# Optimization experiments

Measured on AMD Instinct MI355X. Metric: run time of the kernel, lower is better.

The kernel has to match this reference:

```python
import jax, jax.numpy as jnp
import numpy as np

N = 100000      # nodes
E = 1600000     # edges (no self-loops by construction)
DIN, DH, DOUT = 128, 128, 64
EPS = 1e-8      # torch cosine_similarity eps
LN_EPS = 1e-5


def _segsum(v, idx, n=N):
    return jax.ops.segment_sum(v, idx, num_segments=n)


def att_coef(feats, row, col):
    """Edge-wise cosine-sim attention + degree norm + self-loop append (torch no_grad block).
    Returns fixed-shape (row2, col2, vals2) of length E+N; filtered edges get weight 0
    (equivalent to removal for all scatter_add / message-passing math)."""
    dot = jnp.einsum('ed,ed->e', feats[row], feats[col])            # [E]
    nrm = jnp.maximum(jnp.linalg.norm(feats, axis=1), EPS)          # [N]
    sims = dot / (nrm[row] * nrm[col])
    keep = sims >= 0.1                                              # row!=col guaranteed
    sims = jnp.where(keep, sims, 0.0)
    deg = _segsum(sims, row)
    dinv = jnp.where(deg > 0, deg ** -0.5, 0.0)                     # inf -> 0
    sims = dinv[row] * sims * dinv[col]
    deg_new = _segsum(keep.astype(feats.dtype), col) + 1.0          # [N], >= 1
    self_val = 1.0 / deg_new
    vals = jnp.where(keep, jnp.exp(sims), 0.0)                      # removed edges -> 0
    sl = jnp.arange(N)
    row2 = jnp.concatenate([row, sl])
    col2 = jnp.concatenate([col, sl])
    vals2 = jnp.concatenate([vals, jnp.exp(self_val)])
    return row2, col2, vals2


def gcn_conv(x, row, col, w, W, b):
    """PyG GCNConv (normalize=True, add_self_loops=False) with given edge_weight."""
    h = x @ W                                                        # [N, out]
    deg = _segsum(w, col)
    dinv = jnp.where(deg > 0, deg ** -0.5, 0.0)
    norm = dinv[row] * w * dinv[col]                                 # [E+N]
    out = _segsum(norm[:, None] * h[row], col)                       # scatter to targets
    return out + b


def layer_norm(x, g, b):
    mu = jnp.mean(x, axis=-1, keepdims=True)
    var = jnp.mean((x - mu) ** 2, axis=-1, keepdims=True)
    return (x - mu) * jax.lax.rsqrt(var + LN_EPS) * g + b


def setup_inputs() -> dict:
    key = jax.random.key(0)
    ks = jax.random.split(key, 6)
    x = jax.random.normal(ks[0], (N, DIN), jnp.float32)
    row = jax.random.randint(ks[1], (E,), 0, N)
    col = jax.random.randint(ks[2], (E,), 0, N)
    col = jnp.where(col == row, (col + 1) % N, col)                  # no self-loops
    s1 = float(np.sqrt(6.0 / (DIN + DH)))                            # glorot
    s2 = float(np.sqrt(6.0 / (DH + DOUT)))
    W1 = jax.random.uniform(ks[3], (DIN, DH), jnp.float32, -s1, s1)
    W2 = jax.random.uniform(ks[4], (DH, DOUT), jnp.float32, -s2, s2)
    return dict(x=x, row=row, col=col,
                W1=W1, b1=jnp.zeros((DH,), jnp.float32),
                ln_g=jnp.ones((DH,), jnp.float32), ln_b=jnp.zeros((DH,), jnp.float32),
                W2=W2, b2=jnp.zeros((DOUT,), jnp.float32))


def reference(x, row, col, W1, b1, ln_g, ln_b, W2, b2):
    # layer 1: att_coef (no_grad) -> GCNConv -> LayerNorm -> ReLU (dropout is eval no-op)
    r2, c2, v2 = att_coef(jax.lax.stop_gradient(x), row, col)
    h = gcn_conv(x, r2, c2, v2, W1, b1)
    h = jax.nn.relu(layer_norm(h, ln_g, ln_b))
    # layer 2: att_coef on updated features (original edge list), final conv + log_softmax
    r2, c2, v2 = att_coef(jax.lax.stop_gradient(h), row, col)
    out = gcn_conv(h, r2, c2, v2, W2, b2)
    return jax.nn.log_softmax(out, axis=-1)
```

## Files before the change

kernel.cpp:

```cpp
#include <hip/hip_runtime.h>
#include <math.h>

#define EPSF 1e-8f
#define LN_EPS 1e-5f
#define BL_MARGIN 0.002f

#define BKT_SH 8
#define NBKT 512
#define CHUNK 2048
#define BCAP 5120

typedef unsigned int  u32;
typedef unsigned short u16;
typedef _Float16 h2_t __attribute__((ext_vector_type(2)));
typedef _Float16 half8_t __attribute__((ext_vector_type(8)));
typedef float f32x4_t __attribute__((ext_vector_type(4)));

static __device__ inline u32 pack_h2(float a, float b) {
    h2_t h; h.x = (_Float16)a; h.y = (_Float16)b;
    return __builtin_bit_cast(u32, h);
}
static __device__ inline float h2lo(u32 u) {
    return (float)__builtin_bit_cast(h2_t, u).x;
}
static __device__ inline float h2hi(u32 u) {
    return (float)__builtin_bit_cast(h2_t, u).y;
}

static __device__ inline f32x4_t mfma16(uint4 a, uint4 b, f32x4_t c) {
    return __builtin_amdgcn_mfma_f32_16x16x32_f16(
        __builtin_bit_cast(half8_t, a), __builtin_bit_cast(half8_t, b), c, 0, 0, 0);
}
static __device__ inline float sel4(f32x4_t a, int m) {
    return m == 0 ? a[0] : m == 1 ? a[1] : m == 2 ? a[2] : a[3];
}

__global__ __launch_bounds__(256) void cast_norm_k(const float* __restrict__ feat,
    u32* __restrict__ fhf, float* __restrict__ nrm, float* __restrict__ deg1, int n) {
    int wid  = (blockIdx.x * 256 + threadIdx.x) >> 6;
    int lane = threadIdx.x & 63;
    if (wid >= n) return;
    float2 v = *(const float2*)(feat + (size_t)wid * 128 + lane * 2);
    float s = v.x * v.x + v.y * v.y;
    #pragma unroll
    for (int off = 32; off; off >>= 1) s += __shfl_xor(s, off, 64);
    float nv = fmaxf(sqrtf(s), EPSF);
    float inv = 1.0f / nv;
    fhf[(size_t)wid * 64 + lane] = pack_h2(v.x * inv, v.y * inv);
    if (lane == 0) { nrm[wid] = nv; deg1[wid] = 0.0f; }
}


__global__ __launch_bounds__(256) void binfill_k(const int* __restrict__ row,
    const int* __restrict__ col, int* __restrict__ bcur,
    int2* __restrict__ ebuf, int ecnt) {
    __shared__ int lc[NBKT], ls[NBKT], cur[NBKT], gbase[NBKT];
    __shared__ int2 pairs[CHUNK];
    __shared__ int dstv[CHUNK];
    int t = threadIdx.x;
    int e0 = blockIdx.x * CHUNK;
    int m = min(CHUNK, ecnt - e0);
    lc[t] = 0; lc[t + 256] = 0; cur[t] = 0; cur[t + 256] = 0;
    __syncthreads();
    int myc[CHUNK / 256], myr[CHUNK / 256];
    #pragma unroll
    for (int i = 0; i < CHUNK / 256; ++i) {
        int idx = t + i * 256;
        if (idx < m) {
            myc[i] = col[e0 + idx];
            myr[i] = row[e0 + idx];
            atomicAdd(&lc[myc[i] >> BKT_SH], 1);
        }
    }
    __syncthreads();
    int v0 = lc[t], v1 = lc[t + 256];
    ls[t] = v0; ls[t + 256] = v1; __syncthreads();
    for (int off = 1; off < 256; off <<= 1) {
        int a0 = (t >= off) ? ls[t - off] : 0;
        int a1 = (t >= off) ? ls[256 + t - off] : 0;
        __syncthreads();
        ls[t] += a0; ls[t + 256] += a1;
        __syncthreads();
    }
    int h0 = ls[255];
    int e0x = ls[t] - v0;
    int e1x = ls[t + 256] - v1 + h0;
    __syncthreads();
    ls[t] = e0x; ls[t + 256] = e1x;
    if (v0) gbase[t] = atomicAdd(&bcur[t], v0);
    if (v1) gbase[t + 256] = atomicAdd(&bcur[t + 256], v1);
    __syncthreads();
    #pragma unroll
    for (int i = 0; i < CHUNK / 256; ++i) {
        int idx = t + i * 256;
        if (idx < m) {
            int b = myc[i] >> BKT_SH;
            int s = ls[b] + atomicAdd(&cur[b], 1);
            pairs[s] = make_int2(myc[i], myr[i]);
            int pos = gbase[b] + (s - ls[b]);
            dstv[s]  = (pos < BCAP) ? (b * BCAP + pos) : -1;
        }
    }
    __syncthreads();
    for (int s = t; s < m; s += 256) {
        int d = dstv[s];
        if (d >= 0) ebuf[d] = pairs[s];
    }
}

__global__ __launch_bounds__(256) void bucket_csr_k(const int2* __restrict__ ebuf,
    const int* __restrict__ bcur, int* __restrict__ startAll,
    int* __restrict__ cntAll, int* __restrict__ rowAll, int* __restrict__ colAll,
    int n) {
    __shared__ int sc[NBKT];
    __shared__ int cnt[256], lst[256], cur[256];
    __shared__ int rowbuf[BCAP];
    int b = blockIdx.x, t = threadIdx.x;
    int c0 = b << BKT_SH;
    int s0v = min(bcur[t], BCAP), s1v = min(bcur[t + 256], BCAP);
    sc[t] = s0v; sc[t + 256] = s1v; __syncthreads();
    for (int off = 1; off < 256; off <<= 1) {
        int a0 = (t >= off) ? sc[t - off] : 0;
        int a1 = (t >= off) ? sc[256 + t - off] : 0;
        __syncthreads();
        sc[t] += a0; sc[t + 256] += a1;
        __syncthreads();
    }
    int m  = min(bcur[b], BCAP);
    int g0 = ((b >= 256) ? sc[255] : 0) + sc[b] - m;
    size_t ebase = (size_t)b * BCAP;
    cnt[t] = 0; cur[t] = 0;
    __syncthreads();
    for (int i = t; i < m; i += 256)
        atomicAdd(&cnt[ebuf[ebase + i].x - c0], 1);
    __syncthreads();
    int v = cnt[t];
    lst[t] = v; __syncthreads();
    for (int off = 1; off < 256; off <<= 1) {
        int a = (t >= off) ? lst[t - off] : 0;
        __syncthreads();
        lst[t] += a;
        __syncthreads();
    }
    int ex = lst[t] - v;
    __syncthreads();
    lst[t] = ex;
    __syncthreads();
    int c = c0 + t;
    if (c < n) { startAll[c] = g0 + lst[t]; cntAll[c] = cnt[t]; }
    for (int i = t; i < m; i += 256) {
        int2 p = ebuf[ebase + i];
        int ci = p.x - c0;
        int pos = lst[ci] + atomicAdd(&cur[ci], 1);
        rowbuf[pos] = p.y;
    }
    __syncthreads();
    for (int i = t; i < m; i += 256)
        rowAll[g0 + i] = rowbuf[i];
    __syncthreads();
    {
        int base = lst[t], cn = cnt[t], cc = c0 + t;
        for (int k2 = 0; k2 < cn; ++k2) rowbuf[base + k2] = cc;
    }
    __syncthreads();
    for (int i = t; i < m; i += 256)
        colAll[g0 + i] = rowbuf[i];
}

__global__ __launch_bounds__(256) void edge_dot_flat_k(const u32* __restrict__ fhf,
    const float* __restrict__ feat32, const int* __restrict__ rowAll,
    const int* __restrict__ colAll, const float* __restrict__ nrm,
    float* __restrict__ sims, float* __restrict__ deg1, int ecnt) {
    int wv   = (blockIdx.x * 256 + threadIdx.x) >> 6;
    int lane = threadIdx.x & 63;
    int e0 = wv * 32;
    if (e0 >= ecnt) return;
    int lr = lane & 15, kq = lane >> 4;
    bool diag = (kq == (lr >> 2));
    int m3 = lane & 3;
    int em1 = ecnt - 1;

    int e1 = e0 + lr, e2 = e0 + 16 + lr;
    int e1c = min(e1, em1), e2c = min(e2, em1);
    int r1 = rowAll[e1c], c1 = colAll[e1c];
    int r2 = rowAll[e2c], c2 = colAll[e2c];
    const u32* pa1 = fhf + (size_t)c1 * 64 + kq * 4;
    const u32* pb1 = fhf + (size_t)r1 * 64 + kq * 4;
    const u32* pa2 = fhf + (size_t)c2 * 64 + kq * 4;
    const u32* pb2 = fhf + (size_t)r2 * 64 + kq * 4;
    uint4 a10 = *(const uint4*)(pa1);
    uint4 a11 = *(const uint4*)(pa1 + 16);
    uint4 a12 = *(const uint4*)(pa1 + 32);
    uint4 a13 = *(const uint4*)(pa1 + 48);
    uint4 b10 = *(const uint4*)(pb1);
    uint4 b11 = *(const uint4*)(pb1 + 16);
    uint4 b12 = *(const uint4*)(pb1 + 32);
    uint4 b13 = *(const uint4*)(pb1 + 48);
    uint4 a20 = *(const uint4*)(pa2);
    uint4 a21 = *(const uint4*)(pa2 + 16);
    uint4 a22 = *(const uint4*)(pa2 + 32);
    uint4 a23 = *(const uint4*)(pa2 + 48);
    uint4 b20 = *(const uint4*)(pb2);
    uint4 b21 = *(const uint4*)(pb2 + 16);
    uint4 b22 = *(const uint4*)(pb2 + 32);
    uint4 b23 = *(const uint4*)(pb2 + 48);

    f32x4_t acc1 = {0.f, 0.f, 0.f, 0.f};
    acc1 = mfma16(a10, b10, acc1);
    acc1 = mfma16(a11, b11, acc1);
    acc1 = mfma16(a12, b12, acc1);
    acc1 = mfma16(a13, b13, acc1);
    f32x4_t acc2 = {0.f, 0.f, 0.f, 0.f};
    acc2 = mfma16(a20, b20, acc2);
    acc2 = mfma16(a21, b21, acc2);
    acc2 = mfma16(a22, b22, acc2);
    acc2 = mfma16(a23, b23, acc2);

    float p1 = sel4(acc1, m3);
    float p2 = sel4(acc2, m3);
    bool act1 = diag && (e1 < ecnt);
    bool act2 = diag && (e2 < ecnt);

    unsigned long long bl = __ballot(act1 && fabsf(p1 - 0.1f) < BL_MARGIN);
    while (bl) {
        int src = __ffsll((unsigned long long)bl) - 1; bl &= bl - 1ull;
        int rt = __shfl(r1, src, 64);
        int ct = __shfl(c1, src, 64);
        float2 xa = *(const float2*)(feat32 + (size_t)rt * 128 + lane * 2);
        float2 xb = *(const float2*)(feat32 + (size_t)ct * 128 + lane * 2);
        float s2 = xa.x * xb.x + xa.y * xb.y;
        #pragma unroll
        for (int off = 32; off; off >>= 1) s2 += __shfl_xor(s2, off, 64);
        float pf = s2 / (nrm[rt] * nrm[ct]);
        if (lane == src) p1 = pf;
    }
    unsigned long long bl2 = __ballot(act2 && fabsf(p2 - 0.1f) < BL_MARGIN);
    while (bl2) {
        int src = __ffsll((unsigned long long)bl2) - 1; bl2 &= bl2 - 1ull;
        int rt = __shfl(r2, src, 64);
        int ct = __shfl(c2, src, 64);
        float2 xa = *(const float2*)(feat32 + (size_t)rt * 128 + lane * 2);
        float2 xb = *(const float2*)(feat32 + (size_t)ct * 128 + lane * 2);
        float s2 = xa.x * xb.x + xa.y * xb.y;
        #pragma unroll
        for (int off = 32; off; off >>= 1) s2 += __shfl_xor(s2, off, 64);
        float pf = s2 / (nrm[rt] * nrm[ct]);
        if (lane == src) p2 = pf;
    }
    if (act1) {
        float kv = (p1 >= 0.1f) ? p1 : 0.0f;
        sims[e1] = kv;
        if (kv > 0.0f) atomicAdd(&deg1[r1], kv);
    }
    if (act2) {
        float kv = (p2 >= 0.1f) ? p2 : 0.0f;
        sims[e2] = kv;
        if (kv > 0.0f) atomicAdd(&deg1[r2], kv);
    }
}

__global__ __launch_bounds__(256) void edge_c_csr_k(const float* __restrict__ sims,
    const int* __restrict__ rowAll, const int* __restrict__ startAll,
    const int* __restrict__ cntAll, const float* __restrict__ deg1,
    int2* __restrict__ kv, int* __restrict__ cntK, float* __restrict__ dinv2,
    float* __restrict__ cself, int n) {
    int wid  = (blockIdx.x * 256 + threadIdx.x) >> 6;
    int lane = threadIdx.x & 63;
    if (wid >= n) return;
    int s0 = startAll[wid], cnt = cntAll[wid];
    float degc = deg1[wid];
    float d1c = (degc > 0.0f) ? 1.0f / sqrtf(degc) : 0.0f;
    float vsum = 0.0f; int kc = 0;
    for (int jj = 0; jj < cnt; jj += 64) {
        int j = jj + lane;
        bool keep = false; int r = 0; float v = 0.0f;
        if (j < cnt) {
            float s = sims[s0 + j];
            if (s > 0.0f) {
                r = rowAll[s0 + j];
                float dr = 1.0f / sqrtf(deg1[r]);
                v = expf(dr * s * d1c);
                keep = true;
            }
        }
        unsigned long long m = __ballot(keep ? 1 : 0);
        if (keep) {
            int pre = __popcll(m & ((1ull << lane) - 1ull));
            int2 pk; pk.x = r; pk.y = __float_as_int(v);
            kv[s0 + kc + pre] = pk;
            vsum += v;
        }
        kc += __popcll(m);
    }
    #pragma unroll
    for (int off = 32; off; off >>= 1) vsum += __shfl_xor(vsum, off, 64);
    if (lane == 0) {
        float ws_ = expf(1.0f / ((float)kc + 1.0f));
        float dg = ws_ + vsum;
        float di = 1.0f / sqrtf(dg);
        dinv2[wid] = di;
        cself[wid] = di * ws_;
        cntK[wid]  = kc;
    }
}


__global__ __launch_bounds__(256) void gemm128_k(const float* __restrict__ A,
    const float* __restrict__ W, const float* __restrict__ scale,
    float* __restrict__ out, int n) {
    __shared__ float Ws[128 * 128];
    for (int i = threadIdx.x; i < 128 * 128 / 4; i += 256)
        ((float4*)Ws)[i] = ((const float4*)W)[i];
    __syncthreads();
    const int TPN = 32;
    int group = threadIdx.x / TPN;
    int tin   = threadIdx.x % TPN;
    int nid   = (blockIdx.x * 8 + group) * 4;
    if (nid >= n) return;
    int dbase = tin * 4;
    int nm1 = n - 1;
    const float4* a0 = (const float4*)(A + (size_t)min(nid,     nm1) * 128);
    const float4* a1 = (const float4*)(A + (size_t)min(nid + 1, nm1) * 128);
    const float4* a2 = (const float4*)(A + (size_t)min(nid + 2, nm1) * 128);
    const float4* a3 = (const float4*)(A + (size_t)min(nid + 3, nm1) * 128);
    float4 acc0 = {0,0,0,0}, acc1 = {0,0,0,0}, acc2 = {0,0,0,0}, acc3 = {0,0,0,0};
    #pragma unroll 2
    for (int k4 = 0; k4 < 32; ++k4) {
        const float* wr = Ws + (k4 * 4) * 128 + dbase;
        float4 w0 = *(const float4*)(wr);
        float4 w1 = *(const float4*)(wr + 128);
        float4 w2 = *(const float4*)(wr + 256);
        float4 w3 = *(const float4*)(wr + 384);
        float4 v0 = a0[k4], v1 = a1[k4], v2 = a2[k4], v3 = a3[k4];
        acc0.x += v0.x*w0.x + v0.y*w1.x + v0.z*w2.x + v0.w*w3.x;
        acc0.y += v0.x*w0.y + v0.y*w1.y + v0.z*w2.y + v0.w*w3.y;
        acc0.z += v0.x*w0.z + v0.y*w1.z + v0.z*w2.z + v0.w*w3.z;
        acc0.w += v0.x*w0.w + v0.y*w1.w + v0.z*w2.w + v0.w*w3.w;
        acc1.x += v1.x*w0.x + v1.y*w1.x + v1.z*w2.x + v1.w*w3.x;
        acc1.y += v1.x*w0.y + v1.y*w1.y + v1.z*w2.y + v1.w*w3.y;
        acc1.z += v1.x*w0.z + v1.y*w1.z + v1.z*w2.z + v1.w*w3.z;
        acc1.w += v1.x*w0.w + v1.y*w1.w + v1.z*w2.w + v1.w*w3.w;
        acc2.x += v2.x*w0.x + v2.y*w1.x + v2.z*w2.x + v2.w*w3.x;
        acc2.y += v2.x*w0.y + v2.y*w1.y + v2.z*w2.y + v2.w*w3.y;
        acc2.z += v2.x*w0.z + v2.y*w1.z + v2.z*w2.z + v2.w*w3.z;
        acc2.w += v2.x*w0.w + v2.y*w1.w + v2.z*w2.w + v2.w*w3.w;
        acc3.x += v3.x*w0.x + v3.y*w1.x + v3.z*w2.x + v3.w*w3.x;
        acc3.y += v3.x*w0.y + v3.y*w1.y + v3.z*w2.y + v3.w*w3.y;
        acc3.z += v3.x*w0.z + v3.y*w1.z + v3.z*w2.z + v3.w*w3.z;
        acc3.w += v3.x*w0.w + v3.y*w1.w + v3.z*w2.w + v3.w*w3.w;
    }
    float4 accs[4] = {acc0, acc1, acc2, acc3};
    #pragma unroll
    for (int i = 0; i < 4; ++i) {
        if (nid + i < n) {
            float sc = scale[nid + i];
            float4 r; r.x = accs[i].x * sc; r.y = accs[i].y * sc;
            r.z = accs[i].z * sc; r.w = accs[i].w * sc;
            *(float4*)(out + (size_t)(nid + i) * 128 + dbase) = r;
        }
    }
}

__global__ __launch_bounds__(256) void gemm64_hf_k(const float* __restrict__ A,
    const float* __restrict__ W, const float* __restrict__ scale,
    u32* __restrict__ outhf, int n) {
    __shared__ float Ws[128 * 64];
    for (int i = threadIdx.x; i < 128 * 64 / 4; i += 256)
        ((float4*)Ws)[i] = ((const float4*)W)[i];
    __syncthreads();
    const int TPN = 16;
    int group = threadIdx.x / TPN;
    int tin   = threadIdx.x % TPN;
    int nid   = (blockIdx.x * 16 + group) * 4;
    if (nid >= n) return;
    int dbase = tin * 4;
    int nm1 = n - 1;
    const float4* a0 = (const float4*)(A + (size_t)min(nid,     nm1) * 128);
    const float4* a1 = (const float4*)(A + (size_t)min(nid + 1, nm1) * 128);
    const float4* a2 = (const float4*)(A + (size_t)min(nid + 2, nm1) * 128);
    const float4* a3 = (const float4*)(A + (size_t)min(nid + 3, nm1) * 128);
    float4 acc0 = {0,0,0,0}, acc1 = {0,0,0,0}, acc2 = {0,0,0,0}, acc3 = {0,0,0,0};
    #pragma unroll 2
    for (int k4 = 0; k4 < 32; ++k4) {
        const float* wr = Ws + (k4 * 4) * 64 + dbase;
        float4 w0 = *(const float4*)(wr);
        float4 w1 = *(const float4*)(wr + 64);
        float4 w2 = *(const float4*)(wr + 128);
        float4 w3 = *(const float4*)(wr + 192);
        float4 v0 = a0[k4], v1 = a1[k4], v2 = a2[k4], v3 = a3[k4];
        acc0.x += v0.x*w0.x + v0.y*w1.x + v0.z*w2.x + v0.w*w3.x;
        acc0.y += v0.x*w0.y + v0.y*w1.y + v0.z*w2.y + v0.w*w3.y;
        acc0.z += v0.x*w0.z + v0.y*w1.z + v0.z*w2.z + v0.w*w3.z;
        acc0.w += v0.x*w0.w + v0.y*w1.w + v0.z*w2.w + v0.w*w3.w;
        acc1.x += v1.x*w0.x + v1.y*w1.x + v1.z*w2.x + v1.w*w3.x;
        acc1.y += v1.x*w0.y + v1.y*w1.y + v1.z*w2.y + v1.w*w3.y;
        acc1.z += v1.x*w0.z + v1.y*w1.z + v1.z*w2.z + v1.w*w3.z;
        acc1.w += v1.x*w0.w + v1.y*w1.w + v1.z*w2.w + v1.w*w3.w;
        acc2.x += v2.x*w0.x + v2.y*w1.x + v2.z*w2.x + v2.w*w3.x;
        acc2.y += v2.x*w0.y + v2.y*w1.y + v2.z*w2.y + v2.w*w3.y;
        acc2.z += v2.x*w0.z + v2.y*w1.z + v2.z*w2.z + v2.w*w3.z;
        acc2.w += v2.x*w0.w + v2.y*w1.w + v2.z*w2.w + v2.w*w3.w;
        acc3.x += v3.x*w0.x + v3.y*w1.x + v3.z*w2.x + v3.w*w3.x;
        acc3.y += v3.x*w0.y + v3.y*w1.y + v3.z*w2.y + v3.w*w3.y;
        acc3.z += v3.x*w0.z + v3.y*w1.z + v3.z*w2.z + v3.w*w3.z;
        acc3.w += v3.x*w0.w + v3.y*w1.w + v3.z*w2.w + v3.w*w3.w;
    }
    float4 accs[4] = {acc0, acc1, acc2, acc3};
    #pragma unroll
    for (int i = 0; i < 4; ++i) {
        if (nid + i < n) {
            float sc = scale[nid + i];
            u32 o0 = pack_h2(accs[i].x * sc, accs[i].y * sc);
            u32 o1 = pack_h2(accs[i].z * sc, accs[i].w * sc);
            *(uint2*)(outhf + (size_t)(nid + i) * 32 + tin * 2)
                = make_uint2(o0, o1);
        }
    }
}


__global__ __launch_bounds__(256) void gather_ln_k(const float* __restrict__ hs,
    const int2* __restrict__ kv, const int* __restrict__ startAll,
    const int* __restrict__ cntK, const float* __restrict__ dinv2,
    const float* __restrict__ cself, const float* __restrict__ bias,
    const float* __restrict__ g, const float* __restrict__ bln,
    float* __restrict__ outbuf, u32* __restrict__ outhf,
    float* __restrict__ nrm, float* __restrict__ deg1, int n) {
    int wid = (blockIdx.x * 256 + threadIdx.x) >> 5;
    int l   = threadIdx.x & 31;
    if (wid >= n) return;
    int s0 = startAll[wid], k = cntK[wid];
    if (l == 0) deg1[wid] = 0.0f;
    float4 acc = {0,0,0,0};
    int km1 = s0 + k - 1;
    for (int j0 = 0; j0 < k; j0 += 8) {
        int2 p[8];
        #pragma unroll
        for (int i = 0; i < 8; ++i) p[i] = kv[min(s0 + j0 + i, km1)];
        float4 h[8];
        #pragma unroll
        for (int i = 0; i < 8; ++i)
            h[i] = *(const float4*)(hs + (size_t)p[i].x * 128 + l * 4);
        #pragma unroll
        for (int i = 0; i < 8; ++i) {
            float v = (j0 + i < k) ? __int_as_float(p[i].y) : 0.0f;
            acc.x += v * h[i].x; acc.y += v * h[i].y;
            acc.z += v * h[i].z; acc.w += v * h[i].w;
        }
    }
    float di = dinv2[wid], cs = cself[wid];
    float4 hsv = *(const float4*)(hs + (size_t)wid * 128 + l * 4);
    float4 vb  = *(const float4*)(bias + l * 4);
    float x0 = di*acc.x + cs*hsv.x + vb.x;
    float x1 = di*acc.y + cs*hsv.y + vb.y;
    float x2 = di*acc.z + cs*hsv.z + vb.z;
    float x3 = di*acc.w + cs*hsv.w + vb.w;
    float s = x0 + x1 + x2 + x3;
    #pragma unroll
    for (int off = 16; off; off >>= 1) s += __shfl_xor(s, off, 64);
    float mu = s * (1.0f / 128.0f);
    float d0 = x0 - mu, d1 = x1 - mu, d2 = x2 - mu, d3 = x3 - mu;
    float vv = d0*d0 + d1*d1 + d2*d2 + d3*d3;
    #pragma unroll
    for (int off = 16; off; off >>= 1) vv += __shfl_xor(vv, off, 64);
    float rstd = 1.0f / sqrtf(vv * (1.0f / 128.0f) + LN_EPS);
    float4 vg  = *(const float4*)(g + l * 4);
    float4 vbl = *(const float4*)(bln + l * 4);
    float y0 = fmaxf(d0 * rstd * vg.x + vbl.x, 0.0f);
    float y1 = fmaxf(d1 * rstd * vg.y + vbl.y, 0.0f);
    float y2 = fmaxf(d2 * rstd * vg.z + vbl.z, 0.0f);
    float y3 = fmaxf(d3 * rstd * vg.w + vbl.w, 0.0f);
    float4 yo; yo.x = y0; yo.y = y1; yo.z = y2; yo.w = y3;
    *(float4*)(outbuf + (size_t)wid * 128 + l * 4) = yo;
    float ns = y0*y0 + y1*y1 + y2*y2 + y3*y3;
    #pragma unroll
    for (int off = 16; off; off >>= 1) ns += __shfl_xor(ns, off, 64);
    float nv = fmaxf(sqrtf(ns), EPSF);
    float inv = 1.0f / nv;
    uint2 oh; oh.x = pack_h2(y0 * inv, y1 * inv); oh.y = pack_h2(y2 * inv, y3 * inv);
    *(uint2*)(outhf + (size_t)wid * 64 + l * 2) = oh;
    if (l == 0) nrm[wid] = nv;
}

__global__ __launch_bounds__(256) void gather_lsm_hf_k(const u32* __restrict__ g2s,
    const int2* __restrict__ kv, const int* __restrict__ startAll,
    const int* __restrict__ cntK, const float* __restrict__ dinv2,
    const float* __restrict__ cself, const float* __restrict__ b2,
    float* __restrict__ out, int n) {
    int wid = (blockIdx.x * 256 + threadIdx.x) >> 5;
    int l   = threadIdx.x & 31;
    if (wid >= n) return;
    int s0 = startAll[wid], k = cntK[wid];
    float acc0 = 0.f, acc1 = 0.f;
    int km1 = s0 + k - 1;
    for (int j0 = 0; j0 < k; j0 += 8) {
        int2 p[8];
        #pragma unroll
        for (int i = 0; i < 8; ++i) p[i] = kv[min(s0 + j0 + i, km1)];
        u32 gv[8];
        #pragma unroll
        for (int i = 0; i < 8; ++i) gv[i] = g2s[(size_t)p[i].x * 32 + l];
        #pragma unroll
        for (int i = 0; i < 8; ++i) {
            float v = (j0 + i < k) ? __int_as_float(p[i].y) : 0.0f;
            acc0 += v * h2lo(gv[i]); acc1 += v * h2hi(gv[i]);
        }
    }
    float di = dinv2[wid], cs = cself[wid];
    u32 gsu = g2s[(size_t)wid * 32 + l];
    float2 vb = *(const float2*)(b2 + l * 2);
    float v0 = di * acc0 + cs * h2lo(gsu) + vb.x;
    float v1 = di * acc1 + cs * h2hi(gsu) + vb.y;
    float m = fmaxf(v0, v1);
    #pragma unroll
    for (int off = 16; off; off >>= 1) m = fmaxf(m, __shfl_xor(m, off, 64));
    float e = expf(v0 - m) + expf(v1 - m);
    #pragma unroll
    for (int off = 16; off; off >>= 1) e += __shfl_xor(e, off, 64);
    float lse = m + logf(e);
    *(float2*)(out + (size_t)wid * 64 + l * 2) = make_float2(v0 - lse, v1 - lse);
}


extern "C" void kernel_launch(void* const* d_in, const int* in_sizes, int n_in,
                              void* d_out, int out_size, void* d_ws, size_t ws_size,
                              hipStream_t stream) {
    (void)n_in; (void)out_size; (void)ws_size;
    const float* x   = (const float*)d_in[0];
    const int*   row = (const int*)d_in[1];
    const int*   col = (const int*)d_in[2];
    const float* W1  = (const float*)d_in[3];
    const float* b1  = (const float*)d_in[4];
    const float* lng = (const float*)d_in[5];
    const float* lnb = (const float*)d_in[6];
    const float* W2  = (const float*)d_in[7];
    const float* b2  = (const float*)d_in[8];
    float* out = (float*)d_out;

    const int N = in_sizes[0] / 128;
    const int E = in_sizes[1];

    int*   cntAll   = (int*)d_ws;
    int*   startAll = cntAll + N;
    int*   bcur     = startAll + N;
    float* nrm      = (float*)(bcur + 1024);
    float* deg1     = nrm + N;
    float* dinv2    = deg1 + N;
    float* cself    = dinv2 + N;
    int*   cntK     = (int*)(cself + N);
    int*   rowAll   = cntK + N;
    int*   colAll   = rowAll + E;
    int2*  kvp      = (int2*)(colAll + E);
    u32*   fhf      = (u32*)(kvp + E);
    u32*   g2shf    = fhf + (size_t)64 * N;
    float* big      = (float*)(g2shf + (size_t)32 * N);
    float* sims     = big;
    float* hs       = big;
    float* h2       = big + (size_t)128 * N;
    int2*  ebuf     = (int2*)big;

    const int waveBlocks  = (N + 3) / 4;
    const int halfBlocks  = (N + 7) / 8;
    const int flatBlocks  = (E + 127) / 128;
    const int NB          = (N + 255) >> 8;

    hipMemsetAsync(bcur, 0, NBKT * sizeof(int), stream);
    binfill_k<<<(E + CHUNK - 1) / CHUNK, 256, 0, stream>>>(row, col, bcur, ebuf, E);
    bucket_csr_k<<<NB, 256, 0, stream>>>(ebuf, bcur, startAll, cntAll, rowAll,
                                         colAll, N);

    cast_norm_k<<<waveBlocks, 256, 0, stream>>>(x, fhf, nrm, deg1, N);
    edge_dot_flat_k<<<flatBlocks, 256, 0, stream>>>(fhf, x, rowAll, colAll, nrm,
                                                    sims, deg1, E);
    edge_c_csr_k<<<waveBlocks, 256, 0, stream>>>(sims, rowAll, startAll, cntAll, deg1,
                                                 kvp, cntK, dinv2, cself, N);
    gemm128_k<<<(N + 31) / 32, 256, 0, stream>>>(x, W1, dinv2, hs, N);
    gather_ln_k<<<halfBlocks, 256, 0, stream>>>(hs, kvp, startAll, cntK, dinv2, cself,
                                                b1, lng, lnb, h2, fhf, nrm, deg1, N);

    edge_dot_flat_k<<<flatBlocks, 256, 0, stream>>>(fhf, h2, rowAll, colAll, nrm,
                                                    sims, deg1, E);
    edge_c_csr_k<<<waveBlocks, 256, 0, stream>>>(sims, rowAll, startAll, cntAll, deg1,
                                                 kvp, cntK, dinv2, cself, N);
    gemm64_hf_k<<<(N + 63) / 64, 256, 0, stream>>>(h2, W2, dinv2, g2shf, N);
    gather_lsm_hf_k<<<halfBlocks, 256, 0, stream>>>(g2shf, kvp, startAll, cntK, dinv2,
                                                    cself, b2, out, N);
}
```

Baseline: 603.3 us.

## Co-schedule feature GEMMs with edge-dot kernels and defer source-degree scaling to gathers

Each layer's dense GEMM now runs inside the edge cosine-similarity kernel, with blocks interleaved by a ratio, so the GEMM no longer waits for the degree normalization. Because of that, the per-source dinv scaling is moved out of the GEMM and into the gather kernels, which read dinv2 per neighbor. The interleaved key/value array is split into separate row and weight arrays, with the weights stored in place over sims. The GEMM reads W straight from global/L1 instead of staging it in LDS. The cost is extra per-neighbor dinv loads in the gathers and mixed block types sharing one launch.

```diff
diff --git a/kernel.cpp b/kernel.cpp
--- a/kernel.cpp
+++ b/kernel.cpp
@@ -49,7 +49,6 @@
     fhf[(size_t)wid * 64 + lane] = pack_h2(v.x * inv, v.y * inv);
     if (lane == 0) { nrm[wid] = nv; deg1[wid] = 0.0f; }
 }
-
 
 __global__ __launch_bounds__(256) void binfill_k(const int* __restrict__ row,
     const int* __restrict__ col, int* __restrict__ bcur,
@@ -167,13 +166,12 @@
         colAll[g0 + i] = rowbuf[i];
 }
 
-__global__ __launch_bounds__(256) void edge_dot_flat_k(const u32* __restrict__ fhf,
+static __device__ inline void edge_dot_body(int ewk, const u32* __restrict__ fhf,
     const float* __restrict__ feat32, const int* __restrict__ rowAll,
     const int* __restrict__ colAll, const float* __restrict__ nrm,
     float* __restrict__ sims, float* __restrict__ deg1, int ecnt) {
-    int wv   = (blockIdx.x * 256 + threadIdx.x) >> 6;
     int lane = threadIdx.x & 63;
-    int e0 = wv * 32;
+    int e0 = (ewk * 4 + (int)(threadIdx.x >> 6)) * 32;
     if (e0 >= ecnt) return;
     int lr = lane & 15, kq = lane >> 4;
     bool diag = (kq == (lr >> 2));
@@ -259,63 +257,13 @@
     }
 }
 
-__global__ __launch_bounds__(256) void edge_c_csr_k(const float* __restrict__ sims,
-    const int* __restrict__ rowAll, const int* __restrict__ startAll,
-    const int* __restrict__ cntAll, const float* __restrict__ deg1,
-    int2* __restrict__ kv, int* __restrict__ cntK, float* __restrict__ dinv2,
-    float* __restrict__ cself, int n) {
-    int wid  = (blockIdx.x * 256 + threadIdx.x) >> 6;
-    int lane = threadIdx.x & 63;
-    if (wid >= n) return;
-    int s0 = startAll[wid], cnt = cntAll[wid];
-    float degc = deg1[wid];
-    float d1c = (degc > 0.0f) ? 1.0f / sqrtf(degc) : 0.0f;
-    float vsum = 0.0f; int kc = 0;
-    for (int jj = 0; jj < cnt; jj += 64) {
-        int j = jj + lane;
-        bool keep = false; int r = 0; float v = 0.0f;
-        if (j < cnt) {
-            float s = sims[s0 + j];
-            if (s > 0.0f) {
-                r = rowAll[s0 + j];
-                float dr = 1.0f / sqrtf(deg1[r]);
-                v = expf(dr * s * d1c);
-                keep = true;
-            }
-        }
-        unsigned long long m = __ballot(keep ? 1 : 0);
-        if (keep) {
-            int pre = __popcll(m & ((1ull << lane) - 1ull));
-            int2 pk; pk.x = r; pk.y = __float_as_int(v);
-            kv[s0 + kc + pre] = pk;
-            vsum += v;
-        }
-        kc += __popcll(m);
-    }
-    #pragma unroll
-    for (int off = 32; off; off >>= 1) vsum += __shfl_xor(vsum, off, 64);
-    if (lane == 0) {
-        float ws_ = expf(1.0f / ((float)kc + 1.0f));
-        float dg = ws_ + vsum;
-        float di = 1.0f / sqrtf(dg);
-        dinv2[wid] = di;
-        cself[wid] = di * ws_;
-        cntK[wid]  = kc;
-    }
-}
-
-
-__global__ __launch_bounds__(256) void gemm128_k(const float* __restrict__ A,
-    const float* __restrict__ W, const float* __restrict__ scale,
-    float* __restrict__ out, int n) {
-    __shared__ float Ws[128 * 128];
-    for (int i = threadIdx.x; i < 128 * 128 / 4; i += 256)
-        ((float4*)Ws)[i] = ((const float4*)W)[i];
-    __syncthreads();
+
+static __device__ inline void gemm128_body(int gid, const float* __restrict__ A,
+    const float* __restrict__ W, float* __restrict__ out, int n) {
     const int TPN = 32;
     int group = threadIdx.x / TPN;
     int tin   = threadIdx.x % TPN;
-    int nid   = (blockIdx.x * 8 + group) * 4;
+    int nid   = (gid * 8 + group) * 4;
     if (nid >= n) return;
     int dbase = tin * 4;
     int nm1 = n - 1;
@@ -323,14 +271,14 @@
     const float4* a1 = (const float4*)(A + (size_t)min(nid + 1, nm1) * 128);
     const float4* a2 = (const float4*)(A + (size_t)min(nid + 2, nm1) * 128);
     const float4* a3 = (const float4*)(A + (size_t)min(nid + 3, nm1) * 128);
+    const float4* Wv = (const float4*)W;
     float4 acc0 = {0,0,0,0}, acc1 = {0,0,0,0}, acc2 = {0,0,0,0}, acc3 = {0,0,0,0};
     #pragma unroll 2
     for (int k4 = 0; k4 < 32; ++k4) {
-        const float* wr = Ws + (k4 * 4) * 128 + dbase;
-        float4 w0 = *(const float4*)(wr);
-        float4 w1 = *(const float4*)(wr + 128);
-        float4 w2 = *(const float4*)(wr + 256);
-        float4 w3 = *(const float4*)(wr + 384);
+        float4 w0 = Wv[(k4 * 4 + 0) * 32 + tin];
+        float4 w1 = Wv[(k4 * 4 + 1) * 32 + tin];
+        float4 w2 = Wv[(k4 * 4 + 2) * 32 + tin];
+        float4 w3 = Wv[(k4 * 4 + 3) * 32 + tin];
         float4 v0 = a0[k4], v1 = a1[k4], v2 = a2[k4], v3 = a3[k4];
         acc0.x += v0.x*w0.x + v0.y*w1.x + v0.z*w2.x + v0.w*w3.x;
         acc0.y += v0.x*w0.y + v0.y*w1.y + v0.z*w2.y + v0.w*w3.y;
@@ -352,41 +300,31 @@
     float4 accs[4] = {acc0, acc1, acc2, acc3};
     #pragma unroll
     for (int i = 0; i < 4; ++i) {
-        if (nid + i < n) {
-            float sc = scale[nid + i];
-            float4 r; r.x = accs[i].x * sc; r.y = accs[i].y * sc;
-            r.z = accs[i].z * sc; r.w = accs[i].w * sc;
-            *(float4*)(out + (size_t)(nid + i) * 128 + dbase) = r;
-        }
-    }
-}
-
-__global__ __launch_bounds__(256) void gemm64_hf_k(const float* __restrict__ A,
-    const float* __restrict__ W, const float* __restrict__ scale,
-    u32* __restrict__ outhf, int n) {
-    __shared__ float Ws[128 * 64];
-    for (int i = threadIdx.x; i < 128 * 64 / 4; i += 256)
-        ((float4*)Ws)[i] = ((const float4*)W)[i];
-    __syncthreads();
+        if (nid + i < n)
+            *(float4*)(out + (size_t)(nid + i) * 128 + dbase) = accs[i];
+    }
+}
+
+static __device__ inline void gemm64_body(int gid, const float* __restrict__ A,
+    const float* __restrict__ W, u32* __restrict__ outhf, int n) {
     const int TPN = 16;
     int group = threadIdx.x / TPN;
     int tin   = threadIdx.x % TPN;
-    int nid   = (blockIdx.x * 16 + group) * 4;
+    int nid   = (gid * 16 + group) * 4;
     if (nid >= n) return;
-    int dbase = tin * 4;
     int nm1 = n - 1;
     const float4* a0 = (const float4*)(A + (size_t)min(nid,     nm1) * 128);
     const float4* a1 = (const float4*)(A + (size_t)min(nid + 1, nm1) * 128);
     const float4* a2 = (const float4*)(A + (size_t)min(nid + 2, nm1) * 128);
     const float4* a3 = (const float4*)(A + (size_t)min(nid + 3, nm1) * 128);
+    const float4* Wv = (const float4*)W;
     float4 acc0 = {0,0,0,0}, acc1 = {0,0,0,0}, acc2 = {0,0,0,0}, acc3 = {0,0,0,0};
     #pragma unroll 2
     for (int k4 = 0; k4 < 32; ++k4) {
-        const float* wr = Ws + (k4 * 4) * 64 + dbase;
-        float4 w0 = *(const float4*)(wr);
-        float4 w1 = *(const float4*)(wr + 64);
-        float4 w2 = *(const float4*)(wr + 128);
-        float4 w3 = *(const float4*)(wr + 192);
+        float4 w0 = Wv[(k4 * 4 + 0) * 16 + tin];
+        float4 w1 = Wv[(k4 * 4 + 1) * 16 + tin];
+        float4 w2 = Wv[(k4 * 4 + 2) * 16 + tin];
+        float4 w3 = Wv[(k4 * 4 + 3) * 16 + tin];
         float4 v0 = a0[k4], v1 = a1[k4], v2 = a2[k4], v3 = a3[k4];
         acc0.x += v0.x*w0.x + v0.y*w1.x + v0.z*w2.x + v0.w*w3.x;
         acc0.y += v0.x*w0.y + v0.y*w1.y + v0.z*w2.y + v0.w*w3.y;
@@ -409,18 +347,93 @@
     #pragma unroll
     for (int i = 0; i < 4; ++i) {
         if (nid + i < n) {
-            float sc = scale[nid + i];
-            u32 o0 = pack_h2(accs[i].x * sc, accs[i].y * sc);
-            u32 o1 = pack_h2(accs[i].z * sc, accs[i].w * sc);
+            u32 o0 = pack_h2(accs[i].x, accs[i].y);
+            u32 o1 = pack_h2(accs[i].z, accs[i].w);
             *(uint2*)(outhf + (size_t)(nid + i) * 32 + tin * 2)
                 = make_uint2(o0, o1);
         }
     }
 }
 
+__global__ __launch_bounds__(256) void fused1_k(const u32* __restrict__ fhf,
+    const float* __restrict__ x, const int* __restrict__ rowAll,
+    const int* __restrict__ colAll, const float* __restrict__ nrm,
+    float* __restrict__ sims, float* __restrict__ deg1, int ecnt,
+    const float* __restrict__ W1, float* __restrict__ hs, int n,
+    int R, int nGemm) {
+    int b = blockIdx.x;
+    if ((b % R) == 0 && (b / R) < nGemm) {
+        gemm128_body(b / R, x, W1, hs, n);
+    } else {
+        int e = b - min(b / R + 1, nGemm);
+        edge_dot_body(e, fhf, x, rowAll, colAll, nrm, sims, deg1, ecnt);
+    }
+}
+
+__global__ __launch_bounds__(256) void fused2_k(const u32* __restrict__ h2hf,
+    const float* __restrict__ h2, const int* __restrict__ rowAll,
+    const int* __restrict__ colAll, const float* __restrict__ nrm,
+    float* __restrict__ sims, float* __restrict__ deg1, int ecnt,
+    const float* __restrict__ W2, u32* __restrict__ g2shf, int n,
+    int R, int nGemm) {
+    int b = blockIdx.x;
+    if ((b % R) == 0 && (b / R) < nGemm) {
+        gemm64_body(b / R, h2, W2, g2shf, n);
+    } else {
+        int e = b - min(b / R + 1, nGemm);
+        edge_dot_body(e, h2hf, h2, rowAll, colAll, nrm, sims, deg1, ecnt);
+    }
+}
+
+__global__ __launch_bounds__(256) void edge_c_csr_k(float* __restrict__ simsv,
+    const int* __restrict__ rowAll, const int* __restrict__ startAll,
+    const int* __restrict__ cntAll, const float* __restrict__ deg1,
+    int* __restrict__ krow, int* __restrict__ cntK, float* __restrict__ dinv2,
+    float* __restrict__ cself, int n) {
+    int wid  = (blockIdx.x * 256 + threadIdx.x) >> 6;
+    int lane = threadIdx.x & 63;
+    if (wid >= n) return;
+    int s0 = startAll[wid], cnt = cntAll[wid];
+    float degc = deg1[wid];
+    float d1c = (degc > 0.0f) ? 1.0f / sqrtf(degc) : 0.0f;
+    float vsum = 0.0f; int kc = 0;
+    for (int jj = 0; jj < cnt; jj += 64) {
+        int j = jj + lane;
+        bool keep = false; int r = 0; float v = 0.0f;
+        if (j < cnt) {
+            float s = simsv[s0 + j];
+            if (s > 0.0f) {
+                r = rowAll[s0 + j];
+                float dr = 1.0f / sqrtf(deg1[r]);
+                v = expf(dr * s * d1c);
+                keep = true;
+            }
+        }
+        unsigned long long m = __ballot(keep ? 1 : 0);
+        if (keep) {
+            int pre = __popcll(m & ((1ull << lane) - 1ull));
+            simsv[s0 + kc + pre] = v;
+            krow[s0 + kc + pre] = r;
+            vsum += v;
+        }
+        kc += __popcll(m);
+    }
+    #pragma unroll
+    for (int off = 32; off; off >>= 1) vsum += __shfl_xor(vsum, off, 64);
+    if (lane == 0) {
+        float ws_ = expf(1.0f / ((float)kc + 1.0f));
+        float dg = ws_ + vsum;
+        float di = 1.0f / sqrtf(dg);
+        dinv2[wid] = di;
+        cself[wid] = di * ws_;
+        cntK[wid]  = kc;
+    }
+}
+
 
 __global__ __launch_bounds__(256) void gather_ln_k(const float* __restrict__ hs,
-    const int2* __restrict__ kv, const int* __restrict__ startAll,
+    const int* __restrict__ krow, const float* __restrict__ kval,
+    const int* __restrict__ startAll,
     const int* __restrict__ cntK, const float* __restrict__ dinv2,
     const float* __restrict__ cself, const float* __restrict__ bias,
     const float* __restrict__ g, const float* __restrict__ bln,
@@ -434,21 +447,27 @@
     float4 acc = {0,0,0,0};
     int km1 = s0 + k - 1;
     for (int j0 = 0; j0 < k; j0 += 8) {
-        int2 p[8];
-        #pragma unroll
-        for (int i = 0; i < 8; ++i) p[i] = kv[min(s0 + j0 + i, km1)];
+        int ri[8]; float wv[8];
+        #pragma unroll
+        for (int i = 0; i < 8; ++i) {
+            int idx = min(s0 + j0 + i, km1);
+            ri[i] = krow[idx]; wv[i] = kval[idx];
+        }
+        float dv[8];
+        #pragma unroll
+        for (int i = 0; i < 8; ++i) dv[i] = dinv2[ri[i]];
         float4 h[8];
         #pragma unroll
         for (int i = 0; i < 8; ++i)
-            h[i] = *(const float4*)(hs + (size_t)p[i].x * 128 + l * 4);
+            h[i] = *(const float4*)(hs + (size_t)ri[i] * 128 + l * 4);
         #pragma unroll
         for (int i = 0; i < 8; ++i) {
-            float v = (j0 + i < k) ? __int_as_float(p[i].y) : 0.0f;
-            acc.x += v * h[i].x; acc.y += v * h[i].y;
-            acc.z += v * h[i].z; acc.w += v * h[i].w;
-        }
-    }
-    float di = dinv2[wid], cs = cself[wid];
+            float w = (j0 + i < k) ? wv[i] * dv[i] : 0.0f;
+            acc.x += w * h[i].x; acc.y += w * h[i].y;
+            acc.z += w * h[i].z; acc.w += w * h[i].w;
+        }
+    }
+    float di = dinv2[wid], cs = cself[wid] * di;
     float4 hsv = *(const float4*)(hs + (size_t)wid * 128 + l * 4);
     float4 vb  = *(const float4*)(bias + l * 4);
     float x0 = di*acc.x + cs*hsv.x + vb.x;
@@ -483,7 +502,8 @@
 }
 
 __global__ __launch_bounds__(256) void gather_lsm_hf_k(const u32* __restrict__ g2s,
-    const int2* __restrict__ kv, const int* __restrict__ startAll,
+    const int* __restrict__ krow, const float* __restrict__ kval,
+    const int* __restrict__ startAll,
     const int* __restrict__ cntK, const float* __restrict__ dinv2,
     const float* __restrict__ cself, const float* __restrict__ b2,
     float* __restrict__ out, int n) {
@@ -494,19 +514,25 @@
     float acc0 = 0.f, acc1 = 0.f;
     int km1 = s0 + k - 1;
     for (int j0 = 0; j0 < k; j0 += 8) {
-        int2 p[8];
-        #pragma unroll
-        for (int i = 0; i < 8; ++i) p[i] = kv[min(s0 + j0 + i, km1)];
+        int ri[8]; float wv[8];
+        #pragma unroll
+        for (int i = 0; i < 8; ++i) {
+            int idx = min(s0 + j0 + i, km1);
+            ri[i] = krow[idx]; wv[i] = kval[idx];
+        }
+        float dv[8];
+        #pragma unroll
+        for (int i = 0; i < 8; ++i) dv[i] = dinv2[ri[i]];
         u32 gv[8];
         #pragma unroll
-        for (int i = 0; i < 8; ++i) gv[i] = g2s[(size_t)p[i].x * 32 + l];
+        for (int i = 0; i < 8; ++i) gv[i] = g2s[(size_t)ri[i] * 32 + l];
         #pragma unroll
         for (int i = 0; i < 8; ++i) {
-            float v = (j0 + i < k) ? __int_as_float(p[i].y) : 0.0f;
-            acc0 += v * h2lo(gv[i]); acc1 += v * h2hi(gv[i]);
-        }
-    }
-    float di = dinv2[wid], cs = cself[wid];
+            float w = (j0 + i < k) ? wv[i] * dv[i] : 0.0f;
+            acc0 += w * h2lo(gv[i]); acc1 += w * h2hi(gv[i]);
+        }
+    }
+    float di = dinv2[wid], cs = cself[wid] * di;
     u32 gsu = g2s[(size_t)wid * 32 + l];
     float2 vb = *(const float2*)(b2 + l * 2);
     float v0 = di * acc0 + cs * h2lo(gsu) + vb.x;
@@ -550,11 +576,11 @@
     int*   cntK     = (int*)(cself + N);
     int*   rowAll   = cntK + N;
     int*   colAll   = rowAll + E;
-    int2*  kvp      = (int2*)(colAll + E);
-    u32*   fhf      = (u32*)(kvp + E);
+    float* simsv    = (float*)(colAll + E);
+    int*   krow     = (int*)(simsv + E);
+    u32*   fhf      = (u32*)(krow + E);
     u32*   g2shf    = fhf + (size_t)64 * N;
     float* big      = (float*)(g2shf + (size_t)32 * N);
-    float* sims     = big;
     float* hs       = big;
     float* h2       = big + (size_t)128 * N;
     int2*  ebuf     = (int2*)big;
@@ -564,25 +590,31 @@
     const int flatBlocks  = (E + 127) / 128;
     const int NB          = (N + 255) >> 8;
 
+    const int nGemm1 = (N + 31) / 32;
+    const int tot1   = flatBlocks + nGemm1;
+    const int R1     = tot1 / nGemm1;
+    const int nGemm2 = (N + 63) / 64;
+    const int tot2   = flatBlocks + nGemm2;
+    const int R2     = tot2 / nGemm2;
+
     hipMemsetAsync(bcur, 0, NBKT * sizeof(int), stream);
     binfill_k<<<(E + CHUNK - 1) / CHUNK, 256, 0, stream>>>(row, col, bcur, ebuf, E);
     bucket_csr_k<<<NB, 256, 0, stream>>>(ebuf, bcur, startAll, cntAll, rowAll,
                                          colAll, N);
 
     cast_norm_k<<<waveBlocks, 256, 0, stream>>>(x, fhf, nrm, deg1, N);
-    edge_dot_flat_k<<<flatBlocks, 256, 0, stream>>>(fhf, x, rowAll, colAll, nrm,
-                                                    sims, deg1, E);
-    edge_c_csr_k<<<waveBlocks, 256, 0, stream>>>(sims, rowAll, startAll, cntAll, deg1,
-                                                 kvp, cntK, dinv2, cself, N);
-    gemm128_k<<<(N + 31) / 32, 256, 0, stream>>>(x, W1, dinv2, hs, N);
-    gather_ln_k<<<halfBlocks, 256, 0, stream>>>(hs, kvp, startAll, cntK, dinv2, cself,
-                                                b1, lng, lnb, h2, fhf, nrm, deg1, N);
-
-    edge_dot_flat_k<<<flatBlocks, 256, 0, stream>>>(fhf, h2, rowAll, colAll, nrm,
-                                                    sims, deg1, E);
-    edge_c_csr_k<<<waveBlocks, 256, 0, stream>>>(sims, rowAll, startAll, cntAll, deg1,
-                                                 kvp, cntK, dinv2, cself, N);
-    gemm64_hf_k<<<(N + 63) / 64, 256, 0, stream>>>(h2, W2, dinv2, g2shf, N);
-    gather_lsm_hf_k<<<halfBlocks, 256, 0, stream>>>(g2shf, kvp, startAll, cntK, dinv2,
-                                                    cself, b2, out, N);
-}
+    fused1_k<<<tot1, 256, 0, stream>>>(fhf, x, rowAll, colAll, nrm, simsv, deg1, E,
+                                       W1, hs, N, R1, nGemm1);
+    edge_c_csr_k<<<waveBlocks, 256, 0, stream>>>(simsv, rowAll, startAll, cntAll,
+                                                 deg1, krow, cntK, dinv2, cself, N);
+    gather_ln_k<<<halfBlocks, 256, 0, stream>>>(hs, krow, simsv, startAll, cntK,
+                                                dinv2, cself, b1, lng, lnb,
+                                                h2, fhf, nrm, deg1, N);
+
+    fused2_k<<<tot2, 256, 0, stream>>>(fhf, h2, rowAll, colAll, nrm, simsv, deg1, E,
+                                       W2, g2shf, N, R2, nGemm2);
+    edge_c_csr_k<<<waveBlocks, 256, 0, stream>>>(simsv, rowAll, startAll, cntAll,
+                                                 deg1, krow, cntK, dinv2, cself, N);
+    gather_lsm_hf_k<<<halfBlocks, 256, 0, stream>>>(g2shf, krow, simsv, startAll,
+                                                    cntK, dinv2, cself, b2, out, N);
+}
```

Measured after the change: 872.0 us. 1.45x slower.
